# Optimization experiments

Hardware: AMD Instinct MI355X
Metric: run time of the kernel (lower is better)

## Reference

```python
import jax, jax.numpy as jnp
import numpy as np

B, CF, HH, WW = 32, 768, 28, 28
M, NH = 32, 1024
BETA = 0.05

def _lin(key, out_d, in_d):
    k1, k2 = jax.random.split(key)
    s = 1.0 / np.sqrt(in_d)
    W = jax.random.uniform(k1, (out_d, in_d), minval=-s, maxval=s, dtype=jnp.float32)
    b = jax.random.uniform(k2, (out_d,), minval=-s, maxval=s, dtype=jnp.float32)
    return W, b

def setup_inputs() -> dict:
    key = jax.random.key(0)
    ks = jax.random.split(key, 16)
    inp = {
        'F': jax.random.normal(ks[0], (B, CF, HH, WW), dtype=jnp.float32),
        'A': jax.random.uniform(ks[1], (B, M, HH, WW), dtype=jnp.float32),
        'C': jax.random.normal(ks[2], (1, M * CF), dtype=jnp.float32),
    }
    names = ['xi', 'hi', 'xf', 'hf', 'xo', 'ho', 'xc', 'hc']
    for i, n in enumerate(names):
        in_d = CF if n[0] == 'x' else NH
        W, b = _lin(ks[3 + i], NH, in_d)
        inp['W' + n] = W
        inp['b' + n] = b
    return inp

def reference(F, A, C, Wxi, bxi, Whi, bhi, Wxf, bxf, Whf, bhf, Wxo, bxo, Who, bho, Wxc, bxc, Whc, bhc):
    b = F.shape[0]
    hw = F.shape[2] * F.shape[3]
    m = A.shape[1]
    # BAP: avg-pool of F * A_i over spatial dims, for each attention map -> [B, M, Cf]
    V = jnp.einsum('bchw,bmhw->bmc', F, A) / hw
    V = V.reshape(b, -1)  # [B, M*Cf]
    # RCLoss (center update + detached MSE)
    tmp = jnp.sum(V - C, axis=0)  # [M*Cf]
    C_new = C + (BETA * tmp / b)[None, :]
    diff = jax.lax.stop_gradient(V) - jax.lax.stop_gradient(C_new)
    rcloss = jnp.mean(diff * diff)
    # LSTM over M steps (note: original uses sigmoid for all gates via Sig_i)
    X_seq = V.reshape(b, m, -1).transpose(1, 0, 2)  # [M, B, Cf]
    h0 = jnp.zeros((b, Whi.shape[0]), dtype=V.dtype)
    c0 = jnp.zeros((b, Whi.shape[0]), dtype=V.dtype)
    def step(carry, X):
        H, Cc = carry
        I = jax.nn.sigmoid(X @ Wxi.T + bxi + H @ Whi.T + bhi)
        Fg = jax.nn.sigmoid(X @ Wxf.T + bxf + H @ Whf.T + bhf)
        O = jax.nn.sigmoid(X @ Wxo.T + bxo + H @ Who.T + bho)
        Ct = jnp.tanh(X @ Wxc.T + bxc + H @ Whc.T + bhc)
        Cc = Fg * Cc + I * Ct
        H = O * jnp.tanh(Cc)
        return (H, Cc), None
    (H, _), _ = jax.lax.scan(step, (h0, c0), X_seq)
    return (H, rcloss, C_new)
```

## Files before the change

### kernel.cpp

```cpp
#include <hip/hip_runtime.h>
#include <math.h>

#define CF 768
#define MM 32
#define HW 784
#define MCF 24576
#define BETA 0.05f

typedef __attribute__((ext_vector_type(8))) short bf16x8;
typedef __attribute__((ext_vector_type(4))) float f32x4;

__device__ __forceinline__ unsigned short bf16rne(float x) {
    unsigned int bits = __float_as_uint(x);
    unsigned int r = (bits + 0x7fffu + ((bits >> 16) & 1u)) >> 16;
    return (unsigned short)r;
}
__device__ __forceinline__ float bf2f(unsigned short u) {
    return __uint_as_float(((unsigned int)u) << 16);
}
__device__ __forceinline__ float sigf(float x) { return 1.f / (1.f + __expf(-x)); }
__device__ __forceinline__ float ftanh(float x) {
    x = fminf(fmaxf(x, -12.f), 12.f);
    float e = __expf(2.f * x);
    return (e - 1.f) / (e + 1.f);
}

__device__ __forceinline__ void cvt8(const float4 a, const float4 b, unsigned short* u) {
    u[0] = bf16rne(a.x); u[1] = bf16rne(a.y); u[2] = bf16rne(a.z); u[3] = bf16rne(a.w);
    u[4] = bf16rne(b.x); u[5] = bf16rne(b.y); u[6] = bf16rne(b.z); u[7] = bf16rne(b.w);
}
__device__ __forceinline__ bf16x8 ld_frag(const float* p, bool valid) {
    float4 lo, hi;
    if (valid) { lo = *(const float4*)p; hi = *(const float4*)(p + 4); }
    else { lo = (float4){0,0,0,0}; hi = (float4){0,0,0,0}; }
    unsigned short u[8];
    cvt8(lo, hi, u);
    return *(const bf16x8*)u;
}

__global__ __launch_bounds__(256) void kFE(
    const float* __restrict__ F, const float* __restrict__ Ain,
    unsigned short* __restrict__ Vbf,
    const float* __restrict__ Wxi, const float* __restrict__ Wxf,
    const float* __restrict__ Wxo, const float* __restrict__ Wxc,
    unsigned short* __restrict__ Wxbf,
    const float* __restrict__ Whi, const float* __restrict__ Whf,
    const float* __restrict__ Who, const float* __restrict__ Whc,
    unsigned short* __restrict__ Wbf,
    float* __restrict__ outRC) {
    __shared__ float pls[2][2][64][4];
    const int bid = blockIdx.x;
    const int t = threadIdx.x;

    if (bid >= 768) {
        if (bid == 768 && t == 0) outRC[0] = 0.f;
        if (bid < 2304) {
            int gid = (bid - 768) * 256 + t;
            int row = gid / 96;
            int kq = (gid - row * 96) * 8;
            int g = row >> 10, j = row & 1023;
            const float* Wg = (g == 0) ? Wxi : (g == 1) ? Wxf : (g == 2) ? Wxo : Wxc;
            const float* src = Wg + (size_t)j * CF + kq;
            float4 f0 = *(const float4*)src;
            float4 f1 = *(const float4*)(src + 4);
            unsigned short u[8];
            cvt8(f0, f1, u);
            *(uint4*)&Wxbf[(size_t)row * CF + kq] = *(const uint4*)u;
        } else {
            size_t tid8 = ((size_t)(bid - 2304) * 256 + t) * 8;
            int row = (int)(tid8 >> 10);
            int k = (int)(tid8 & 1023);
            int g = row >> 10, j = row & 1023;
            const float* Wg = (g == 0) ? Whi : (g == 1) ? Whf : (g == 2) ? Who : Whc;
            const float* src = Wg + (size_t)j * 1024 + k;
            float4 f0 = *(const float4*)src;
            float4 f1 = *(const float4*)(src + 4);
            unsigned short u[8];
            cvt8(f0, f1, u);
            *(uint4*)&Wbf[tid8] = *(const uint4*)u;
        }
        return;
    }

    const int b = bid / 24, ct = bid - b * 24;
    const int cbase = ct * 32;
    const int lane = t & 63, w = t >> 6;
    const int cw = w & 1, kh = w >> 1;
    const int n = lane & 15, q = lane >> 4;

    const float* Arow0 = Ain + ((size_t)(b * 32 + n)) * HW;
    const float* Arow1 = Ain + ((size_t)(b * 32 + 16 + n)) * HW;
    const float* Frow  = F + ((size_t)(b * CF) + cbase + cw * 16 + n) * HW;
    const int kq8 = q * 8;

    f32x4 acc0 = {0.f, 0.f, 0.f, 0.f};
    f32x4 acc1 = {0.f, 0.f, 0.f, 0.f};

    #pragma unroll 4
    for (int kc = 0; kc < 13; ++kc) {
        const int k = (kh * 13 + kc) * 32 + kq8;
        const bool valid = (k < HW);
        bf16x8 bf_ = ld_frag(Frow + k, valid);
        bf16x8 a0 = ld_frag(Arow0 + k, valid);
        bf16x8 a1 = ld_frag(Arow1 + k, valid);
        acc0 = __builtin_amdgcn_mfma_f32_16x16x32_bf16(a0, bf_, acc0, 0, 0, 0);
        acc1 = __builtin_amdgcn_mfma_f32_16x16x32_bf16(a1, bf_, acc1, 0, 0, 0);
    }

    if (kh == 1) {
        #pragma unroll
        for (int r = 0; r < 4; ++r) {
            pls[cw][0][lane][r] = acc0[r];
            pls[cw][1][lane][r] = acc1[r];
        }
    }
    __syncthreads();
    if (kh == 0) {
        #pragma unroll
        for (int r = 0; r < 4; ++r) {
            acc0[r] += pls[cw][0][lane][r];
            acc1[r] += pls[cw][1][lane][r];
        }
        #pragma unroll
        for (int r = 0; r < 4; ++r) {
            int m0 = q * 4 + r;
            Vbf[(size_t)(b * 32 + m0) * CF + cbase + cw * 16 + n] =
                bf16rne(acc0[r] * (1.f / 784.f));
            Vbf[(size_t)(b * 32 + 16 + m0) * CF + cbase + cw * 16 + n] =
                bf16rne(acc1[r] * (1.f / 784.f));
        }
    }
}

__global__ __launch_bounds__(512) void kC3B(
    const unsigned short* __restrict__ Vbf,
    const unsigned short* __restrict__ Wxbf,
    const float* __restrict__ bxi, const float* __restrict__ bxf,
    const float* __restrict__ bxo, const float* __restrict__ bxc,
    const float* __restrict__ bhi, const float* __restrict__ bhf,
    const float* __restrict__ bho, const float* __restrict__ bhc,
    unsigned short* __restrict__ Xbf,
    const float* __restrict__ C, float* __restrict__ Cnew_out,
    float* __restrict__ outRC) {
    __shared__ unsigned short Asg[512 * 8];
    const int bx = blockIdx.x;
    const int by = blockIdx.y;
    const int t = threadIdx.x;

    if (bx >= 16) {
        int e = (bx - 16) * 32 + by;
        if (e < 48) {
            int j = e * 512 + t;
            float c = C[j];
            float s = 0.f;
            #pragma unroll 4
            for (int b = 0; b < 32; ++b) s += bf2f(Vbf[(size_t)b * MCF + j]);
            float cn = c + BETA * (s * (1.f / 32.f) - c);
            Cnew_out[j] = cn;
            float ds = 0.f;
            #pragma unroll 4
            for (int b = 0; b < 32; ++b) {
                float d = bf2f(Vbf[(size_t)b * MCF + j]) - cn;
                ds = fmaf(d, d, ds);
            }
            float* red = (float*)Asg;
            red[t] = ds;
            __syncthreads();
            for (int off = 256; off > 0; off >>= 1) {
                if (t < off) red[t] += red[t + off];
                __syncthreads();
            }
            if (t == 0) atomicAdd(outRC, red[0] * (1.f / (32.f * 24576.f)));
        }
        return;
    }

    const int lane = t & 63;
    const int w = t >> 6;
    const int n = lane & 15;
    const int q = lane >> 4;
    const int mbase = bx * 64;

    const int st_row = (w & 3) * 16 + n;
    const int st_kb  = (w >> 2) * 4 + q;
    const int st_rg  = mbase + st_row;
    const int st_vrow = (st_rg & 31) * 32 + (st_rg >> 5);
    const unsigned short* st_src = Vbf + (size_t)st_vrow * CF + st_kb * 8;

    const int nb = by * 128 + w * 16;
    const unsigned short* Brow = Wxbf + (size_t)(nb + n) * CF + q * 8;

    f32x4 acc[4];
    #pragma unroll
    for (int g = 0; g < 4; ++g) acc[g] = (f32x4){0.f, 0.f, 0.f, 0.f};

    uint4 st = *(const uint4*)st_src;
    for (int kc = 0; kc < 12; ++kc) {
        __syncthreads();
        *(uint4*)&Asg[t * 8] = st;
        __syncthreads();
        if (kc + 1 < 12) st = *(const uint4*)(st_src + (kc + 1) * 64);
        #pragma unroll
        for (int p = 0; p < 2; ++p) {
            bf16x8 bfr = *(const bf16x8*)(Brow + kc * 64 + p * 32);
            #pragma unroll
            for (int g = 0; g < 4; ++g) {
                bf16x8 a = *(const bf16x8*)&Asg[((p * 4 + g) * 64 + lane) * 8];
                acc[g] = __builtin_amdgcn_mfma_f32_16x16x32_bf16(a, bfr, acc[g], 0, 0, 0);
            }
        }
    }

    const int gg = by >> 3;
    const int j = (by & 7) * 128 + w * 16 + n;
    const float* bx_ = (gg == 0) ? bxi : (gg == 1) ? bxf : (gg == 2) ? bxo : bxc;
    const float* bh_ = (gg == 0) ? bhi : (gg == 1) ? bhf : (gg == 2) ? bho : bhc;
    const float bias = bx_[j] + bh_[j];
    #pragma unroll
    for (int g = 0; g < 4; ++g) {
        #pragma unroll
        for (int rr = 0; rr < 4; ++rr) {
            int rg = mbase + g * 16 + q * 4 + rr;
            int tt = rg >> 5, bb = rg & 31;
            Xbf[((size_t)(tt * 4 + gg) * 32 + bb) * 1024 + j] = bf16rne(acc[g][rr] + bias);
        }
    }
}

__global__ __launch_bounds__(512) void kStep(
    const unsigned short* __restrict__ Wbf,
    const unsigned short* __restrict__ Xbf,
    const unsigned short* __restrict__ Hprev,
    unsigned short* __restrict__ Hnext,
    float* __restrict__ Cst,
    float* __restrict__ outH,
    int step) {
    __shared__ float pbuf[8][32][17];
    __shared__ float sbuf[32][17];
    const int bi = blockIdx.x;
    const int jbase = bi * 4;
    const int t = threadIdx.x;
    const int lane = t & 63;
    const int w = t >> 6;
    const int n = lane & 15;
    const int q = lane >> 4;

    const int pb = t >> 4, pnn = t & 15;
    const int pg = pnn >> 2, pjj = pnn & 3;
    const float xv = bf2f(Xbf[(((size_t)step * 4 + pg) * 32 + pb) * 1024 + jbase + pjj]);
    float cprev = 0.f;
    if (step > 0 && t < 128) cprev = Cst[(t >> 2) * 1024 + jbase + (t & 3)];

    if (step > 0) {
        const int g = n >> 2, jj = n & 3;
        const unsigned short* Wrow = Wbf + ((size_t)(g * 1024 + jbase + jj)) * 1024 + w * 128;
        const unsigned short* hb0 = Hprev + (size_t)n * 1024 + w * 128;
        const unsigned short* hb1 = Hprev + (size_t)(n + 16) * 1024 + w * 128;
        f32x4 acc0 = {0.f, 0.f, 0.f, 0.f};
        f32x4 acc1 = {0.f, 0.f, 0.f, 0.f};
        #pragma unroll
        for (int ks = 0; ks < 4; ++ks) {
            int k = ks * 32 + q * 8;
            bf16x8 bfrag = *(const bf16x8*)(Wrow + k);
            bf16x8 a0 = *(const bf16x8*)(hb0 + k);
            bf16x8 a1 = *(const bf16x8*)(hb1 + k);
            acc0 = __builtin_amdgcn_mfma_f32_16x16x32_bf16(a0, bfrag, acc0, 0, 0, 0);
            acc1 = __builtin_amdgcn_mfma_f32_16x16x32_bf16(a1, bfrag, acc1, 0, 0, 0);
        }
        #pragma unroll
        for (int r = 0; r < 4; ++r) {
            pbuf[w][q * 4 + r][n] = acc0[r];
            pbuf[w][16 + q * 4 + r][n] = acc1[r];
        }
    }
    __syncthreads();
    {
        float s = xv;
        if (step > 0) {
            #pragma unroll
            for (int w2 = 0; w2 < 8; ++w2) s += pbuf[w2][pb][pnn];
        }
        sbuf[pb][pnn] = s;
    }
    __syncthreads();
    if (t < 128) {
        int b = t >> 2, jj = t & 3;
        float I  = sigf(sbuf[b][jj]);
        float Fg = sigf(sbuf[b][4 + jj]);
        float O  = sigf(sbuf[b][8 + jj]);
        float Ct = ftanh(sbuf[b][12 + jj]);
        float c = fmaf(Fg, cprev, I * Ct);
        Cst[b * 1024 + jbase + jj] = c;
        float h = O * ftanh(c);
        if (step < 31) {
            Hnext[b * 1024 + jbase + jj] = bf16rne(h);
        } else {
            outH[b * 1024 + jbase + jj] = h;
        }
    }
}

extern "C" void kernel_launch(void* const* d_in, const int* in_sizes, int n_in,
                              void* d_out, int out_size, void* d_ws, size_t ws_size,
                              hipStream_t stream) {
    const float* F   = (const float*)d_in[0];
    const float* A   = (const float*)d_in[1];
    const float* C   = (const float*)d_in[2];
    const float* Wxi = (const float*)d_in[3];
    const float* bxi = (const float*)d_in[4];
    const float* Whi = (const float*)d_in[5];
    const float* bhi = (const float*)d_in[6];
    const float* Wxf = (const float*)d_in[7];
    const float* bxf = (const float*)d_in[8];
    const float* Whf = (const float*)d_in[9];
    const float* bhf = (const float*)d_in[10];
    const float* Wxo = (const float*)d_in[11];
    const float* bxo = (const float*)d_in[12];
    const float* Who = (const float*)d_in[13];
    const float* bho = (const float*)d_in[14];
    const float* Wxc = (const float*)d_in[15];
    const float* bxc = (const float*)d_in[16];
    const float* Whc = (const float*)d_in[17];
    const float* bhc = (const float*)d_in[18];

    float* out   = (float*)d_out;
    float* outH  = out;
    float* outRC = out + 32768;
    float* outC  = out + 32769;

    float* ws = (float*)d_ws;
    unsigned short* Xbf  = (unsigned short*)ws;
    unsigned short* Wxbf = (unsigned short*)(ws + 2097152);
    unsigned short* Wbf  = (unsigned short*)(ws + 3670016);
    unsigned short* Vbf  = (unsigned short*)(ws + 5767168);
    unsigned short* Hbf  = (unsigned short*)(ws + 6160384);
    float* Cst  = ws + 6193152;

    kFE<<<dim3(4352), 256, 0, stream>>>(F, A, Vbf,
                                        Wxi, Wxf, Wxo, Wxc, Wxbf,
                                        Whi, Whf, Who, Whc, Wbf, outRC);
    kC3B<<<dim3(18, 32), 512, 0, stream>>>(Vbf, Wxbf,
                                           bxi, bxf, bxo, bxc,
                                           bhi, bhf, bho, bhc, Xbf,
                                           C, outC, outRC);

    for (int step = 0; step < 32; ++step) {
        const unsigned short* Hprev = Hbf + ((step + 1) & 1) * 32768;
        unsigned short* Hnext = (unsigned short*)(Hbf + (step & 1) * 32768);
        kStep<<<dim3(256), 512, 0, stream>>>(Wbf, Xbf, Hprev, Hnext, Cst, outH, step);
    }
}
```

Measured before the change: 236.4 us.

## Software-pipeline BAP loads with inline-asm triple buffering and packed bf16 convert

Rewrites the BAP MFMA loop as a hand-scheduled triple-buffered pipeline using inline-asm global loads with immediate offsets and explicit vmcnt waits, so loads overlap the convert and MFMA work. The K split between the two wave halves changes from contiguous halves to interleaved 32-element chunks, with a tail chunk handled separately. The software bf16 rounding is replaced by the hardware v_cvt_pk_bf16_f32 instruction. This adds register pressure and relies on hand-managed waitcnt correctness.

```diff
diff --git a/kernel.cpp b/kernel.cpp
--- a/kernel.cpp
+++ b/kernel.cpp
@@ -10,6 +10,8 @@
 typedef __attribute__((ext_vector_type(8))) short bf16x8;
 typedef __attribute__((ext_vector_type(4))) float f32x4;
 
+typedef union { unsigned int u[4]; bf16x8 v; } pk8u;
+
 __device__ __forceinline__ unsigned short bf16rne(float x) {
     unsigned int bits = __float_as_uint(x);
     unsigned int r = (bits + 0x7fffu + ((bits >> 16) & 1u)) >> 16;
@@ -24,18 +26,14 @@
     float e = __expf(2.f * x);
     return (e - 1.f) / (e + 1.f);
 }
-
 __device__ __forceinline__ void cvt8(const float4 a, const float4 b, unsigned short* u) {
     u[0] = bf16rne(a.x); u[1] = bf16rne(a.y); u[2] = bf16rne(a.z); u[3] = bf16rne(a.w);
     u[4] = bf16rne(b.x); u[5] = bf16rne(b.y); u[6] = bf16rne(b.z); u[7] = bf16rne(b.w);
 }
-__device__ __forceinline__ bf16x8 ld_frag(const float* p, bool valid) {
-    float4 lo, hi;
-    if (valid) { lo = *(const float4*)p; hi = *(const float4*)(p + 4); }
-    else { lo = (float4){0,0,0,0}; hi = (float4){0,0,0,0}; }
-    unsigned short u[8];
-    cvt8(lo, hi, u);
-    return *(const bf16x8*)u;
+__device__ __forceinline__ unsigned int cvtpk(float lo, float hi) {
+    unsigned int r;
+    asm("v_cvt_pk_bf16_f32 %0, %1, %2" : "=v"(r) : "v"(lo), "v"(hi));
+    return r;
 }
 
 __global__ __launch_bounds__(256) void kFE(
@@ -88,23 +86,76 @@
     const int cw = w & 1, kh = w >> 1;
     const int n = lane & 15, q = lane >> 4;
 
-    const float* Arow0 = Ain + ((size_t)(b * 32 + n)) * HW;
-    const float* Arow1 = Ain + ((size_t)(b * 32 + 16 + n)) * HW;
-    const float* Frow  = F + ((size_t)(b * CF) + cbase + cw * 16 + n) * HW;
-    const int kq8 = q * 8;
+    const float* pF  = F + ((size_t)(b * CF) + cbase + cw * 16 + n) * HW + kh * 32 + q * 8;
+    const float* pA0 = Ain + ((size_t)(b * 32 + n)) * HW + kh * 32 + q * 8;
+    const float* pA1 = Ain + ((size_t)(b * 32 + 16 + n)) * HW + kh * 32 + q * 8;
 
     f32x4 acc0 = {0.f, 0.f, 0.f, 0.f};
     f32x4 acc1 = {0.f, 0.f, 0.f, 0.f};
 
-    #pragma unroll 4
-    for (int kc = 0; kc < 13; ++kc) {
-        const int k = (kh * 13 + kc) * 32 + kq8;
-        const bool valid = (k < HW);
-        bf16x8 bf_ = ld_frag(Frow + k, valid);
-        bf16x8 a0 = ld_frag(Arow0 + k, valid);
-        bf16x8 a1 = ld_frag(Arow1 + k, valid);
-        acc0 = __builtin_amdgcn_mfma_f32_16x16x32_bf16(a0, bf_, acc0, 0, 0, 0);
-        acc1 = __builtin_amdgcn_mfma_f32_16x16x32_bf16(a1, bf_, acc1, 0, 0, 0);
+    float4 bufA[6], bufB[6], bufC[6];
+
+#define ISSUE(BUF, IMM)                                                                   \
+    asm volatile("global_load_dwordx4 %0, %1, off offset:%2" : "=v"(BUF[0]) : "v"(pF),  "n"(IMM));      \
+    asm volatile("global_load_dwordx4 %0, %1, off offset:%2" : "=v"(BUF[1]) : "v"(pF),  "n"(IMM + 16)); \
+    asm volatile("global_load_dwordx4 %0, %1, off offset:%2" : "=v"(BUF[2]) : "v"(pA0), "n"(IMM));      \
+    asm volatile("global_load_dwordx4 %0, %1, off offset:%2" : "=v"(BUF[3]) : "v"(pA0), "n"(IMM + 16)); \
+    asm volatile("global_load_dwordx4 %0, %1, off offset:%2" : "=v"(BUF[4]) : "v"(pA1), "n"(IMM));      \
+    asm volatile("global_load_dwordx4 %0, %1, off offset:%2" : "=v"(BUF[5]) : "v"(pA1), "n"(IMM + 16));
+
+#define WAITP(N)                                              \
+    asm volatile("s_waitcnt vmcnt(" #N ")" ::: "memory");     \
+    __builtin_amdgcn_sched_barrier(0);
+
+#define COMPP(BUF)                                                          \
+    {                                                                       \
+        pk8u uf_, u0_, u1_;                                                 \
+        uf_.u[0] = cvtpk(BUF[0].x, BUF[0].y); uf_.u[1] = cvtpk(BUF[0].z, BUF[0].w); \
+        uf_.u[2] = cvtpk(BUF[1].x, BUF[1].y); uf_.u[3] = cvtpk(BUF[1].z, BUF[1].w); \
+        u0_.u[0] = cvtpk(BUF[2].x, BUF[2].y); u0_.u[1] = cvtpk(BUF[2].z, BUF[2].w); \
+        u0_.u[2] = cvtpk(BUF[3].x, BUF[3].y); u0_.u[3] = cvtpk(BUF[3].z, BUF[3].w); \
+        u1_.u[0] = cvtpk(BUF[4].x, BUF[4].y); u1_.u[1] = cvtpk(BUF[4].z, BUF[4].w); \
+        u1_.u[2] = cvtpk(BUF[5].x, BUF[5].y); u1_.u[3] = cvtpk(BUF[5].z, BUF[5].w); \
+        acc0 = __builtin_amdgcn_mfma_f32_16x16x32_bf16(u0_.v, uf_.v, acc0, 0, 0, 0); \
+        acc1 = __builtin_amdgcn_mfma_f32_16x16x32_bf16(u1_.v, uf_.v, acc1, 0, 0, 0); \
+    }
+
+    ISSUE(bufA, 0);
+    ISSUE(bufB, 256);
+    ISSUE(bufC, 512);  WAITP(12); COMPP(bufA);
+    ISSUE(bufA, 768);  WAITP(12); COMPP(bufB);
+    ISSUE(bufB, 1024); WAITP(12); COMPP(bufC);
+    ISSUE(bufC, 1280); WAITP(12); COMPP(bufA);
+    ISSUE(bufA, 1536); WAITP(12); COMPP(bufB);
+    ISSUE(bufB, 1792); WAITP(12); COMPP(bufC);
+    ISSUE(bufC, 2048); WAITP(12); COMPP(bufA);
+    ISSUE(bufA, 2304); WAITP(12); COMPP(bufB);
+    ISSUE(bufB, 2560); WAITP(12); COMPP(bufC);
+    ISSUE(bufC, 2816); WAITP(12); COMPP(bufA);
+    WAITP(6);  COMPP(bufB);
+    WAITP(0);  COMPP(bufC);
+
+#undef ISSUE
+#undef WAITP
+#undef COMPP
+
+    if (kh == 0) {
+        float4 tz = {0.f, 0.f, 0.f, 0.f};
+        float4 tb[6] = {tz, tz, tz, tz, tz, tz};
+        if (q < 2) {
+            tb[0] = *(const float4*)(pF + 768);  tb[1] = *(const float4*)(pF + 772);
+            tb[2] = *(const float4*)(pA0 + 768); tb[3] = *(const float4*)(pA0 + 772);
+            tb[4] = *(const float4*)(pA1 + 768); tb[5] = *(const float4*)(pA1 + 772);
+        }
+        pk8u uf_, u0_, u1_;
+        uf_.u[0] = cvtpk(tb[0].x, tb[0].y); uf_.u[1] = cvtpk(tb[0].z, tb[0].w);
+        uf_.u[2] = cvtpk(tb[1].x, tb[1].y); uf_.u[3] = cvtpk(tb[1].z, tb[1].w);
+        u0_.u[0] = cvtpk(tb[2].x, tb[2].y); u0_.u[1] = cvtpk(tb[2].z, tb[2].w);
+        u0_.u[2] = cvtpk(tb[3].x, tb[3].y); u0_.u[3] = cvtpk(tb[3].z, tb[3].w);
+        u1_.u[0] = cvtpk(tb[4].x, tb[4].y); u1_.u[1] = cvtpk(tb[4].z, tb[4].w);
+        u1_.u[2] = cvtpk(tb[5].x, tb[5].y); u1_.u[3] = cvtpk(tb[5].z, tb[5].w);
+        acc0 = __builtin_amdgcn_mfma_f32_16x16x32_bf16(u0_.v, uf_.v, acc0, 0, 0, 0);
+        acc1 = __builtin_amdgcn_mfma_f32_16x16x32_bf16(u1_.v, uf_.v, acc1, 0, 0, 0);
     }
 
     if (kh == 1) {
```

Measured after the change: 237.2 us. Within noise of the previous version (+0.4%).
